# Kernel tuning notes

Measured on AMD Instinct MI355X. Metric: run time of the kernel, lower is better.

Reference implementation:

```python
import jax, jax.numpy as jnp
import numpy as np

D_MODEL = 1024
D_INNER = 2048      # expand * d_model
D_STATE = 64
HEADDIM = 128
NHEADS = 16         # d_inner // headdim
D_CONV = 4
CHUNK = 256
D_IN_PROJ = 2 * D_INNER + 2 * D_STATE + NHEADS   # 4240 (ngroups=1)
CONV_DIM = D_INNER + 2 * D_STATE                 # 2176
EPS = 1e-5


def setup_inputs() -> dict:
    key = jax.random.key(0)
    ks = jax.random.split(key, 8)
    B, L = 2, 4096
    u = jax.random.normal(ks[0], (B, L, D_MODEL), jnp.float32)
    in_proj_w = jax.random.normal(ks[1], (D_IN_PROJ, D_MODEL), jnp.float32) / np.sqrt(D_MODEL)
    conv_w = jax.random.uniform(ks[2], (CONV_DIM, D_CONV), jnp.float32, -0.5, 0.5)
    conv_b = jnp.zeros((CONV_DIM,), jnp.float32)
    # dt_bias init exactly as in the module: inv-softplus of dt ~ logU(1e-3, 1e-1)
    dt0 = jnp.exp(jax.random.uniform(ks[3], (NHEADS,), jnp.float32) * (np.log(0.1) - np.log(0.001)) + np.log(0.001))
    dt_bias = dt0 + jnp.log(-jnp.expm1(-dt0))
    A_log = jnp.log(jax.random.uniform(ks[4], (NHEADS,), jnp.float32, 1.0, 16.0))
    Dp = jnp.ones((NHEADS,), jnp.float32)
    norm_w = jnp.ones((D_INNER,), jnp.float32)
    out_proj_w = jax.random.normal(ks[5], (D_MODEL, D_INNER), jnp.float32) / np.sqrt(D_INNER)
    return dict(u=u, in_proj_w=in_proj_w, conv_w=conv_w, conv_b=conv_b, dt_bias=dt_bias,
                A_log=A_log, Dp=Dp, norm_w=norm_w, out_proj_w=out_proj_w)


def _ssd(x, dt, A, Bm, Cm, Dp):
    # Chunked selective state-space scan (mamba_chunk_scan_combined semantics).
    # x: [b,l,h,p], dt: [b,l,h] (already softplus'd), A: [h] (negative), Bm/Cm: [b,l,n]
    b, l, h, p = x.shape
    n = Bm.shape[-1]
    nc = l // CHUNK
    xc = x.reshape(b, nc, CHUNK, h, p)
    dtc = dt.reshape(b, nc, CHUNK, h)
    Bc = Bm.reshape(b, nc, CHUNK, n)
    Cc = Cm.reshape(b, nc, CHUNK, n)
    a = dtc * A                       # [b,c,q,h], a <= 0
    acum = jnp.cumsum(a, axis=2)      # within-chunk cumulative log-decay
    # ---- intra-chunk (causal, attention-like) ----
    scores = jnp.einsum('bcqn,bckn->bcqk', Cc, Bc)
    diff = acum[:, :, :, None, :] - acum[:, :, None, :, :]        # [b,c,q,k,h]
    mask = jnp.tril(jnp.ones((CHUNK, CHUNK), bool))[None, None, :, :, None]
    decay = jnp.exp(jnp.where(mask, diff, -jnp.inf))
    M = scores[..., None] * decay * dtc[:, :, None, :, :]         # [b,c,q,k,h]
    y_diag = jnp.einsum('bcqkh,bckhp->bcqhp', M, xc)
    # ---- per-chunk end states ----
    decay_states = jnp.exp(acum[:, :, -1:, :] - acum)             # [b,c,q,h]
    states = jnp.einsum('bcqh,bcqn,bcqhp->bchpn', dtc * decay_states, Bc, xc)
    # ---- inter-chunk recurrence (scan over nc chunks) ----
    chunk_decay = jnp.exp(acum[:, :, -1, :])                      # [b,c,h]
    def step(s, inp):
        st, cd = inp
        return cd[:, :, None, None] * s + st, s                   # emit state BEFORE this chunk
    init = jnp.zeros((b, h, p, n), x.dtype)
    _, prev = jax.lax.scan(step, init, (states.transpose(1, 0, 2, 3, 4), chunk_decay.transpose(1, 0, 2)))
    prev = prev.transpose(1, 0, 2, 3, 4)                          # [b,c,h,p,n]
    y_off = jnp.einsum('bcqn,bchpn,bcqh->bcqhp', Cc, prev, jnp.exp(acum))
    y = y_diag + y_off + xc * Dp[None, None, None, :, None]
    return y.reshape(b, l, h, p)


def _forward(u, in_proj_w, conv_w, conv_b, dt_bias, A_log, Dp, norm_w, out_proj_w):
    b, l, _ = u.shape
    zxbct = jnp.einsum('bld,ed->ble', u, in_proj_w)
    z = zxbct[..., :D_INNER]
    xBC = zxbct[..., D_INNER:D_INNER + CONV_DIM]
    dt = zxbct[..., D_INNER + CONV_DIM:]
    dt = jax.nn.softplus(dt + dt_bias)                            # [b,l,h]
    # causal depthwise conv1d (padding d_conv-1, truncated to seq_len) + SiLU
    xp = jnp.pad(xBC, ((0, 0), (D_CONV - 1, 0), (0, 0)))
    conv_out = conv_b
    for w in range(D_CONV):
        conv_out = conv_out + xp[:, w:w + l, :] * conv_w[:, w]
    xBC = jax.nn.silu(conv_out)
    x = xBC[..., :D_INNER]
    Bm = xBC[..., D_INNER:D_INNER + D_STATE]
    Cm = xBC[..., D_INNER + D_STATE:]
    A = -jnp.exp(A_log)
    y = _ssd(x.reshape(b, l, NHEADS, HEADDIM), dt, A, Bm, Cm, Dp)
    y = y.reshape(b, l, D_INNER)
    # RMSNormGated (norm_before_gate=False): gate first, then RMSNorm
    y = y * jax.nn.silu(z)
    y = y * jax.lax.rsqrt(jnp.mean(y * y, axis=-1, keepdims=True) + EPS) * norm_w
    return jnp.einsum('ble,de->bld', y, out_proj_w)


def reference(u, in_proj_w, conv_w, conv_b, dt_bias, A_log, Dp, norm_w, out_proj_w):
    return _forward(u, in_proj_w, conv_w, conv_b, dt_bias, A_log, Dp, norm_w, out_proj_w)
```

## Files before the change

kernel.cpp:

```cpp
#include <hip/hip_runtime.h>
#include <hip/hip_bf16.h>
#include <cstdint>
#include <cstddef>

#define D_MODEL   1024
#define D_INNER   2048
#define D_STATE   64
#define HEADDIM   128
#define NHEADS    16
#define D_CONV    4
#define CHUNK     256
#define D_IN_PROJ 4240
#define ZPAD      4352
#define CONV_DIM  2176
#define NB        2
#define LEN       4096
#define NC        16
#define MROWS     (NB*LEN)

typedef __hip_bfloat16 bf16;
typedef __bf16 bf16x8 __attribute__((ext_vector_type(8)));
typedef float  f32x4  __attribute__((ext_vector_type(4)));
typedef unsigned short us4 __attribute__((ext_vector_type(4)));

__device__ __forceinline__ float fsilu(float x){ return x / (1.f + __expf(-x)); }
__device__ __forceinline__ float toF(float x){ return x; }
__device__ __forceinline__ float toF(bf16 x){ return __bfloat162float(x); }

__device__ __forceinline__ unsigned short f2bs(float v){
  return __bfloat16_as_ushort(__float2bfloat16(v));
}
__device__ __forceinline__ void store4(bf16* p, f32x4 v){
  us4 o; o[0]=f2bs(v[0]); o[1]=f2bs(v[1]); o[2]=f2bs(v[2]); o[3]=f2bs(v[3]);
  *(us4*)p = o;
}
__device__ __forceinline__ void store4(float* p, f32x4 v){
  *(f32x4*)p = v;
}

__device__ __forceinline__ void gload_lds16(const void* g, void* l){
  __builtin_amdgcn_global_load_lds(
     (const __attribute__((address_space(1))) unsigned int*)(uintptr_t)g,
     (__attribute__((address_space(3))) unsigned int*)(uintptr_t)l, 16, 0, 0);
}

template<typename TC>
__global__ __launch_bounds__(512) void k_gemm_8w(
    const bf16* __restrict__ A, int lda,
    const bf16* __restrict__ B, int ldb,
    TC* __restrict__ C, int ldc, int K)
{
  __shared__ __align__(16) __bf16 As[2][128*64];
  __shared__ __align__(16) __bf16 Bs[2][128*64];
  const int tid  = threadIdx.x;
  const int w    = tid >> 6, l = tid & 63;
  const int quad = l >> 4, lq = l & 15;
  const int wm   = (w & 1)*64;
  const int wn   = (w >> 1)*32;
  const int m0 = blockIdx.x*128, n0 = blockIdx.y*128;

  const int sr = tid >> 3;
  const int sc = ((tid & 7) ^ (sr & 7)) * 8;
  const bf16* Ag = A + (size_t)(m0 + sr)*lda + sc;
  const bf16* Bg = B + (size_t)(n0 + sr)*ldb + sc;
  const int sdo = w*1024;

  auto stage = [&](int t, int buf){
    const int k0 = t*64;
    char* ab = (char*)&As[buf][0] + sdo;
    char* bb = (char*)&Bs[buf][0] + sdo;
    gload_lds16(Ag + k0,                  ab);
    gload_lds16(Ag + (size_t)64*lda + k0, ab + 8192);
    gload_lds16(Bg + k0,                  bb);
    gload_lds16(Bg + (size_t)64*ldb + k0, bb + 8192);
  };

  f32x4 acc[4][2] = {};

  stage(0, 0);
  const int NT = K >> 6;
  for (int t = 0; t < NT; ++t){
    const int cur = t & 1;
    if (t+1 < NT){
      stage(t+1, cur^1);
      asm volatile("s_waitcnt vmcnt(4)" ::: "memory");
    } else {
      asm volatile("s_waitcnt vmcnt(0)" ::: "memory");
    }
    asm volatile("s_barrier" ::: "memory");

    const char* Ab = (const char*)&As[cur][0];
    const char* Bb = (const char*)&Bs[cur][0];
    #pragma unroll
    for (int s=0;s<2;s++){
      const int slot = (((s*4 + quad) ^ (lq & 7)) << 4);
      bf16x8 af[4], bfr[2];
      #pragma unroll
      for (int tm=0;tm<4;tm++)
        af[tm]  = *(const bf16x8*)(Ab + (wm + tm*16 + lq)*128 + slot);
      #pragma unroll
      for (int tn=0;tn<2;tn++)
        bfr[tn] = *(const bf16x8*)(Bb + (wn + tn*16 + lq)*128 + slot);
      #pragma unroll
      for (int tm=0;tm<4;tm++)
        #pragma unroll
        for (int tn=0;tn<2;tn++)
          acc[tm][tn] = __builtin_amdgcn_mfma_f32_16x16x32_bf16(bfr[tn], af[tm], acc[tm][tn], 0,0,0);
    }
    asm volatile("s_barrier" ::: "memory");
  }

  #pragma unroll
  for (int tm = 0; tm < 4; tm++){
    int r = m0 + wm + tm*16 + lq;
    #pragma unroll
    for (int tn = 0; tn < 2; tn++){
      int cb = n0 + wn + tn*16 + quad*4;
      store4(&C[(size_t)r*ldc + cb], acc[tm][tn]);
    }
  }
}

template<typename TC>
__global__ __launch_bounds__(256) void k_gemm_db(
    const bf16* __restrict__ A, int lda,
    const bf16* __restrict__ B, int ldb,
    TC* __restrict__ C, int ldc, int K)
{
  __shared__ __align__(16) __bf16 As[2][128*64];
  __shared__ __align__(16) __bf16 Bs[2][128*64];
  const int tid  = threadIdx.x;
  const int w    = tid >> 6, l = tid & 63;
  const int quad = l >> 4, lq = l & 15;
  const int wm   = (w & 1)*64, wn = (w >> 1)*64;
  const int m0 = blockIdx.x*128, n0 = blockIdx.y*128;

  const int rs = w*8 + (l >> 3);
  const int cs = ((l & 7) ^ (l >> 3)) * 8;
  const bf16* Ag = A + (size_t)(m0 + rs)*lda + cs;
  const bf16* Bg = B + (size_t)(n0 + rs)*ldb + cs;

  auto stage = [&](int t, int buf){
    const int k0 = t*64;
    #pragma unroll
    for (int j=0;j<4;j++){
      gload_lds16(Ag + (size_t)j*32*lda + k0, (char*)&As[buf][0] + (j*32 + w*8)*128);
      gload_lds16(Bg + (size_t)j*32*ldb + k0, (char*)&Bs[buf][0] + (j*32 + w*8)*128);
    }
  };

  f32x4 acc[4][4] = {};

  stage(0, 0);
  const int NT = K >> 6;
  for (int t = 0; t < NT; ++t){
    const int cur = t & 1;
    if (t+1 < NT){
      stage(t+1, cur^1);
      asm volatile("s_waitcnt vmcnt(8)" ::: "memory");
    } else {
      asm volatile("s_waitcnt vmcnt(0)" ::: "memory");
    }
    asm volatile("s_barrier" ::: "memory");

    const char* Ab = (const char*)&As[cur][0];
    const char* Bb = (const char*)&Bs[cur][0];
    #pragma unroll
    for (int s=0;s<2;s++){
      const int slot = ((s*4 + quad) ^ (lq & 7)) << 4;
      bf16x8 af[4], bfr[4];
      #pragma unroll
      for (int tm=0;tm<4;tm++)
        af[tm]  = *(const bf16x8*)(Ab + (wm + lq + tm*16)*128 + slot);
      #pragma unroll
      for (int tn=0;tn<4;tn++)
        bfr[tn] = *(const bf16x8*)(Bb + (wn + lq + tn*16)*128 + slot);
      #pragma unroll
      for (int tm=0;tm<4;tm++)
        #pragma unroll
        for (int tn=0;tn<4;tn++)
          acc[tm][tn] = __builtin_amdgcn_mfma_f32_16x16x32_bf16(bfr[tn], af[tm], acc[tm][tn], 0,0,0);
    }
    asm volatile("s_barrier" ::: "memory");
  }

  #pragma unroll
  for (int tm = 0; tm < 4; tm++){
    int r = m0 + wm + tm*16 + lq;
    #pragma unroll
    for (int tn = 0; tn < 4; tn++){
      int cb = n0 + wn + tn*16 + quad*4;
      store4(&C[(size_t)r*ldc + cb], acc[tm][tn]);
    }
  }
}

#define NU4  (MROWS*D_MODEL/4)
#define NW14 (ZPAD*D_MODEL/4)
#define NW24 (D_MODEL*D_INNER/4)
__global__ __launch_bounds__(256) void k_convert(
    const float* __restrict__ u, const float* __restrict__ Win,
    const float* __restrict__ Wout, const float* __restrict__ norm_w,
    bf16* __restrict__ ub, bf16* __restrict__ Wb_in, bf16* __restrict__ Wb_out){
  int i4 = blockIdx.x*256 + threadIdx.x;
  if (i4 < NU4){
    float4 v = ((const float4*)u)[i4];
    us4 o = {f2bs(v.x), f2bs(v.y), f2bs(v.z), f2bs(v.w)};
    ((us4*)ub)[i4] = o;
  } else if (i4 < NU4 + NW14){
    int j = i4 - NU4;
    int r = j >> 8;
    float4 v = make_float4(0.f,0.f,0.f,0.f);
    if (r < D_IN_PROJ) v = ((const float4*)Win)[j];
    us4 o = {f2bs(v.x), f2bs(v.y), f2bs(v.z), f2bs(v.w)};
    ((us4*)Wb_in)[j] = o;
  } else {
    int j = i4 - NU4 - NW14;
    float4 v = ((const float4*)Wout)[j];
    float4 nw = ((const float4*)norm_w)[j & 511];
    us4 o = {f2bs(v.x*nw.x), f2bs(v.y*nw.y), f2bs(v.z*nw.z), f2bs(v.w*nw.w)};
    ((us4*)Wb_out)[j] = o;
  }
}

__global__ __launch_bounds__(256) void k_dt(
    const bf16* __restrict__ zxbct, const float* __restrict__ dt_bias,
    const float* __restrict__ A_log, float* __restrict__ dt_t,
    float* __restrict__ acum_t, float* __restrict__ cd_t){
  int bid = blockIdx.x;
  int h = bid & 15, c = (bid>>4)&15, b = bid>>8;
  int q = threadIdx.x;
  size_t m = (size_t)(b*NC + c)*CHUNK + q;
  float x = toF(zxbct[m*ZPAD + (D_INNER + CONV_DIM) + h]) + dt_bias[h];
  float dtv = (x > 20.f) ? x : log1pf(__expf(x));
  float Ah = -__expf(A_log[h]);
  float a = dtv * Ah;
  __shared__ float sb[CHUNK];
  sb[q] = a;
  __syncthreads();
  #pragma unroll
  for (int off=1; off<CHUNK; off<<=1){
    float t = (q >= off) ? sb[q-off] : 0.f;
    __syncthreads();
    sb[q] += t;
    __syncthreads();
  }
  float ac = sb[q];
  size_t o = ((size_t)(b*NHEADS+h))*LEN + c*CHUNK + q;
  dt_t[o]   = dtv;
  acum_t[o] = ac;
  if (q == CHUNK-1) cd_t[(b*NHEADS+h)*NC + c] = __expf(ac);
}

__global__ __launch_bounds__(256) void k_conv(
    const bf16* __restrict__ zxbct, const float* __restrict__ conv_w,
    const float* __restrict__ conv_b, bf16* __restrict__ xbc){
  __shared__ __align__(16) __bf16 xs[67*64];
  __shared__ __align__(16) float  ws[64*4];
  __shared__ float bs[64];
  const int tid = threadIdx.x;
  const int cq = tid & 7;
  const int tm = tid >> 3;
  const int c0 = blockIdx.x*64;
  const int m0 = blockIdx.y*64;
  {
    int g = m0 - 3 + tm; if (g < 0) g = 0;
    *(bf16x8*)&xs[tm*64 + cq*8] =
        *(const bf16x8*)(zxbct + (size_t)g*ZPAD + D_INNER + c0 + cq*8);
    int g2 = m0 - 3 + tm + 32;
    *(bf16x8*)&xs[(tm+32)*64 + cq*8] =
        *(const bf16x8*)(zxbct + (size_t)g2*ZPAD + D_INNER + c0 + cq*8);
    if (tid < 24){
      int r3 = 64 + (tid >> 3);
      int g3 = m0 - 3 + r3;
      *(bf16x8*)&xs[r3*64 + cq*8] =
          *(const bf16x8*)(zxbct + (size_t)g3*ZPAD + D_INNER + c0 + cq*8);
    }
  }
  if (tid < 64)      *(float4*)&ws[tid*4] = *(const float4*)(conv_w + (size_t)(c0+tid)*4);
  else if (tid < 128) bs[tid-64] = conv_b[c0 + tid - 64];
  __syncthreads();

  #pragma unroll
  for (int rr=0; rr<2; rr++){
    const int r = tm + rr*32;
    const int m = m0 + r;
    const int l = m & (LEN-1);
    float acc[8];
    #pragma unroll
    for (int j=0;j<8;j++) acc[j] = bs[cq*8+j];
    #pragma unroll
    for (int w=0; w<D_CONV; w++){
      if (l - (D_CONV-1) + w >= 0){
        bf16x8 v = *(const bf16x8*)&xs[(r+w)*64 + cq*8];
        #pragma unroll
        for (int j=0;j<8;j++) acc[j] += (float)v[j] * ws[(cq*8+j)*4 + w];
      }
    }
    bf16x8 o;
    #pragma unroll
    for (int j=0;j<8;j++) o[j] = (__bf16)fsilu(acc[j]);
    *(bf16x8*)(xbc + (size_t)m*CONV_DIM + c0 + cq*8) = o;
  }
}

__global__ __launch_bounds__(256,2) void k_states(
    const bf16* __restrict__ xbc, const float* __restrict__ acum_t,
    const float* __restrict__ dt_t, float* __restrict__ states)
{
  const int bid = blockIdx.x;
  const int h = bid & 15, c = (bid>>4)&15, b = bid>>8;
  const int z = b*NC + c;
  const int tid = threadIdx.x;
  const int w = tid >> 6, l = tid & 63;
  const int quad = l >> 4, lq = l & 15;

  __shared__ __align__(16) __bf16 xsT[2][128*72];
  __shared__ __align__(16) __bf16 bts[2][64*72];

  const float* acum = acum_t + ((size_t)(b*NHEADS+h))*LEN + c*CHUNK;
  const float* dtc  = dt_t   + ((size_t)(b*NHEADS+h))*LEN + c*CHUNK;
  const float alast = acum[CHUNK-1];
  const bf16* xrow = xbc + (size_t)z*CHUNK*CONV_DIM + h*HEADDIM;
  const bf16* Brow = xbc + (size_t)z*CHUNK*CONV_DIM + D_INNER;

  f32x4 Sst[2][4] = {};

  auto stage = [&](int t, int buf){
    const int k0 = t*64;
    const bf16* xr = xrow + (size_t)(k0+l)*CONV_DIM;
    #pragma unroll
    for (int pass=0; pass<4; pass++){
      int pb = w*8 + pass*32;
      bf16x8 v = *(const bf16x8*)(xr + pb);
      #pragma unroll
      for (int j=0;j<8;j++) xsT[buf][(pb+j)*72 + l] = v[j];
    }
    float wl = dtc[k0+l] * __expf(alast - acum[k0+l]);
    const bf16* br = Brow + (size_t)(k0+l)*CONV_DIM;
    #pragma unroll
    for (int pass=0; pass<2; pass++){
      int nb = w*8 + pass*32;
      bf16x8 v = *(const bf16x8*)(br + nb);
      #pragma unroll
      for (int j=0;j<8;j++) bts[buf][(nb+j)*72 + l] = (__bf16)((float)v[j] * wl);
    }
  };

  stage(0, 0);
  for (int t = 0; t < 4; t++){
    const int buf = t & 1;
    __syncthreads();
    if (t < 3) stage(t+1, buf^1);
    #pragma unroll
    for (int s=0;s<2;s++){
      bf16x8 a2[2];
      #pragma unroll
      for (int mi=0;mi<2;mi++)
        a2[mi] = *(const bf16x8*)&xsT[buf][(w*32 + mi*16 + lq)*72 + s*32 + quad*8];
      #pragma unroll
      for (int ni=0;ni<4;ni++){
        bf16x8 bb = *(const bf16x8*)&bts[buf][(ni*16+lq)*72 + s*32 + quad*8];
        #pragma unroll
        for (int mi=0;mi<2;mi++)
          Sst[mi][ni] = __builtin_amdgcn_mfma_f32_16x16x32_bf16(bb, a2[mi], Sst[mi][ni], 0,0,0);
      }
    }
  }

  float* so = states + (size_t)bid*HEADDIM*D_STATE;
  #pragma unroll
  for (int mi=0;mi<2;mi++){
    int pp = w*32 + mi*16 + lq;
    #pragma unroll
    for (int ni=0;ni<4;ni++)
      store4(&so[pp*D_STATE + ni*16 + quad*4], Sst[mi][ni]);
  }
}

__global__ __launch_bounds__(256) void k_scan(
    const float* __restrict__ states, const float* __restrict__ cd_t,
    bf16* __restrict__ prevb){
  int b = blockIdx.x >> 4, h = blockIdx.x & 15;
  int pt = blockIdx.y;
  int tid = threadIdx.x;
  float carry[4] = {0.f,0.f,0.f,0.f};
  for (int c=0;c<NC;c++){
    size_t base = ((size_t)(b*256 + c*16 + h))*HEADDIM*D_STATE + (size_t)pt*1024;
    float cd = cd_t[(b*NHEADS+h)*NC + c];
    #pragma unroll
    for (int i=0;i<4;i++){
      size_t idx = base + (size_t)i*256 + tid;
      prevb[idx] = __float2bfloat16(carry[i]);
      carry[i] = carry[i]*cd + states[idx];
    }
  }
}

__global__ __launch_bounds__(256,2) void k_fused(
    const bf16* __restrict__ xbc, const float* __restrict__ acum_t,
    const float* __restrict__ dt_t, const float* __restrict__ Dp,
    const bf16* __restrict__ prevb, bf16* __restrict__ y)
{
  const int bid = blockIdx.x;
  const int h = bid & 15, c = (bid>>4)&15, b = bid>>8;
  const int z = b*NC + c;
  const int tid = threadIdx.x;
  const int w = tid >> 6, l = tid & 63;
  const int quad = l >> 4, lq = l & 15;

  __shared__ __align__(16) __bf16 xsT[2][128*72];
  __shared__ __align__(16) __bf16 Ms[4][32*40];
  __shared__ float acs[CHUNK], dts[CHUNK];

  const float* acum = acum_t + ((size_t)(b*NHEADS+h))*LEN + c*CHUNK;
  const float* dtc  = dt_t   + ((size_t)(b*NHEADS+h))*LEN + c*CHUNK;
  acs[tid] = acum[tid];
  dts[tid] = dtc[tid];

  const bf16* xrow = xbc + (size_t)z*CHUNK*CONV_DIM + h*HEADDIM;
  const bf16* Brow = xbc + (size_t)z*CHUNK*CONV_DIM + D_INNER;
  const bf16* Crow = xbc + (size_t)z*CHUNK*CONV_DIM + D_INNER + D_STATE;
  const bf16* pv   = prevb + (size_t)bid*HEADDIM*D_STATE;
  const float Dph = Dp[h];
  const int j0 = w, j1 = 7 - w;

  f32x4 Yacc[2][2][8] = {};

  auto stage = [&](int t, int buf){
    const bf16* xr = xrow + (size_t)(t*64+l)*CONV_DIM;
    #pragma unroll
    for (int pass=0; pass<4; pass++){
      int pb = w*8 + pass*32;
      bf16x8 v = *(const bf16x8*)(xr + pb);
      #pragma unroll
      for (int j=0;j<8;j++) xsT[buf][(pb+j)*72 + l] = v[j];
    }
  };

  stage(0, 0);
  __syncthreads();

  #pragma unroll
  for (int s=0;s<2;s++){
    bf16x8 bp[8];
    #pragma unroll
    for (int pn=0;pn<8;pn++)
      bp[pn] = *(const bf16x8*)(pv + (pn*16+lq)*D_STATE + s*32 + quad*8);
    #pragma unroll
    for (int half=0; half<2; half++){
      const int j = half ? j1 : j0;
      #pragma unroll
      for (int qm=0;qm<2;qm++){
        int row = j*32 + qm*16 + lq;
        float e = __expf(acs[row]);
        bf16x8 a = *(const bf16x8*)(Crow + (size_t)row*CONV_DIM + s*32 + quad*8);
        bf16x8 ae;
        #pragma unroll
        for (int jj=0;jj<8;jj++) ae[jj] = (__bf16)((float)a[jj] * e);
        #pragma unroll
        for (int pn=0;pn<8;pn++)
          Yacc[half][qm][pn] = __builtin_amdgcn_mfma_f32_16x16x32_bf16(bp[pn], ae, Yacc[half][qm][pn], 0,0,0);
      }
    }
  }

  for (int t = 0; t < 4; t++){
    const int buf = t & 1;
    if (t > 0) __syncthreads();
    if (t < 3) stage(t+1, buf^1);

    #pragma unroll
    for (int half=0; half<2; half++){
      const int j = half ? j1 : j0;
      if (2*t > j) continue;
      const int qbase = j*32;
      bf16x8 cf[2][2];
      #pragma unroll
      for (int s=0;s<2;s++)
        #pragma unroll
        for (int qm=0;qm<2;qm++)
          cf[s][qm] = *(const bf16x8*)(Crow + (size_t)(qbase+qm*16+lq)*CONV_DIM + s*32 + quad*8);
      #pragma unroll
      for (int kk=0; kk<2; kk++){
        const int kh = 2*t + kk;
        if (kh > j) continue;
        const int kb32  = kk*32;
        const int kbase = kh*32;
        f32x4 Sacc[2][2] = {};
        #pragma unroll
        for (int s=0;s<2;s++){
          bf16x8 bfk[2];
          #pragma unroll
          for (int kn=0;kn<2;kn++)
            bfk[kn] = *(const bf16x8*)(Brow + (size_t)(kbase+kn*16+lq)*CONV_DIM + s*32 + quad*8);
          #pragma unroll
          for (int kn=0;kn<2;kn++)
            #pragma unroll
            for (int qm=0;qm<2;qm++)
              Sacc[kn][qm] = __builtin_amdgcn_mfma_f32_16x16x32_bf16(bfk[kn], cf[s][qm], Sacc[kn][qm], 0,0,0);
        }
        #pragma unroll
        for (int qm=0;qm<2;qm++){
          int ql = qbase + qm*16 + lq;
          float aq = acs[ql];
          #pragma unroll
          for (int kn=0;kn<2;kn++){
            us4 o;
            #pragma unroll
            for (int i=0;i<4;i++){
              int kl = kbase + kn*16 + quad*4 + i;
              float v = Sacc[kn][qm][i] * __expf(aq - acs[kl]) * dts[kl];
              v = (kl < ql) ? v : ((kl == ql) ? v + Dph : 0.f);
              o[i] = f2bs(v);
            }
            *(us4*)&Ms[w][(qm*16+lq)*40 + kn*16 + quad*4] = o;
          }
        }
        asm volatile("s_waitcnt lgkmcnt(0)" ::: "memory");
        #pragma unroll
        for (int qm=0;qm<2;qm++){
          bf16x8 am = *(const bf16x8*)&Ms[w][(qm*16+lq)*40 + quad*8];
          #pragma unroll
          for (int pn=0;pn<8;pn++){
            bf16x8 bp = *(const bf16x8*)&xsT[buf][(pn*16+lq)*72 + kb32 + quad*8];
            Yacc[half][qm][pn] = __builtin_amdgcn_mfma_f32_16x16x32_bf16(bp, am, Yacc[half][qm][pn], 0,0,0);
          }
        }
      }
    }
  }

  bf16* yrow = y + (size_t)z*CHUNK*D_INNER + h*HEADDIM;
  #pragma unroll
  for (int half=0; half<2; half++){
    const int j = half ? j1 : j0;
    #pragma unroll
    for (int qm=0;qm<2;qm++){
      int q = j*32 + qm*16 + lq;
      #pragma unroll
      for (int pn=0;pn<8;pn++)
        store4(&yrow[(size_t)q*D_INNER + pn*16 + quad*4], Yacc[half][qm][pn]);
    }
  }
}

__global__ __launch_bounds__(256) void k_gatenorm(
    const bf16* __restrict__ zxbct, bf16* __restrict__ y){
  int m = blockIdx.x;
  int e0 = threadIdx.x*8;
  bf16x8 zv = *(const bf16x8*)(zxbct + (size_t)m*ZPAD + e0);
  bf16x8 yv = *(const bf16x8*)(y + (size_t)m*D_INNER + e0);
  float v[8]; float ss = 0.f;
  #pragma unroll
  for (int j=0;j<8;j++){
    float val = (float)yv[j] * fsilu((float)zv[j]);
    v[j] = val; ss += val*val;
  }
  #pragma unroll
  for (int off=32; off>0; off>>=1) ss += __shfl_down(ss, off, 64);
  __shared__ float red[4];
  if ((threadIdx.x & 63) == 0) red[threadIdx.x >> 6] = ss;
  __syncthreads();
  float tot = red[0]+red[1]+red[2]+red[3];
  float r = rsqrtf(tot * (1.f/D_INNER) + 1e-5f);
  bf16x8 o;
  #pragma unroll
  for (int j=0;j<8;j++) o[j] = (__bf16)(v[j] * r);
  *(bf16x8*)(y + (size_t)m*D_INNER + e0) = o;
}

extern "C" void kernel_launch(void* const* d_in, const int* in_sizes, int n_in,
                              void* d_out, int out_size, void* d_ws, size_t ws_size,
                              hipStream_t stream) {
  const float* u         = (const float*)d_in[0];
  const float* in_proj_w = (const float*)d_in[1];
  const float* conv_w    = (const float*)d_in[2];
  const float* conv_b    = (const float*)d_in[3];
  const float* dt_bias   = (const float*)d_in[4];
  const float* A_log     = (const float*)d_in[5];
  const float* Dp        = (const float*)d_in[6];
  const float* norm_w    = (const float*)d_in[7];
  const float* out_proj_w= (const float*)d_in[8];
  float* out = (float*)d_out;

  char* p = (char*)d_ws;
  auto alloc = [&](size_t bytes){ char* r = p; p += (bytes + 255) & ~size_t(255); return r; };
  bf16*  zxbct = (bf16*) alloc((size_t)MROWS*ZPAD*2);
  bf16*  xbc   = (bf16*) alloc((size_t)MROWS*CONV_DIM*2);
  bf16*  y     = (bf16*) alloc((size_t)MROWS*D_INNER*2);
  bf16*  ub    = (bf16*) alloc((size_t)MROWS*D_MODEL*2);
  bf16*  Wb_in = (bf16*) alloc((size_t)ZPAD*D_MODEL*2);
  bf16*  Wb_out= (bf16*) alloc((size_t)D_MODEL*D_INNER*2);
  float* dt_t  = (float*)alloc((size_t)NB*NHEADS*LEN*4);
  float* acum_t= (float*)alloc((size_t)NB*NHEADS*LEN*4);
  float* cd_t  = (float*)alloc((size_t)NB*NHEADS*NC*4);
  float* states= (float*)ub;
  bf16*  prevb = (bf16*)Wb_in;

  dim3 blk(256);
  k_convert<<<dim3((NU4+NW14+NW24)/256), blk, 0, stream>>>(
      u, in_proj_w, out_proj_w, norm_w, ub, Wb_in, Wb_out);

  k_gemm_8w<bf16><<<dim3(64, 34), dim3(512), 0, stream>>>(
      ub, D_MODEL, Wb_in, D_MODEL, zxbct, ZPAD, D_MODEL);

  k_dt    <<<dim3(NB*NC*NHEADS), blk, 0, stream>>>(zxbct, dt_bias, A_log, dt_t, acum_t, cd_t);
  k_conv  <<<dim3(CONV_DIM/64, MROWS/64), blk, 0, stream>>>(zxbct, conv_w, conv_b, xbc);
  k_states<<<dim3(NB*NC*NHEADS), blk, 0, stream>>>(xbc, acum_t, dt_t, states);
  k_scan  <<<dim3(NB*NHEADS, 8), blk, 0, stream>>>(states, cd_t, prevb);
  k_fused <<<dim3(NB*NC*NHEADS), blk, 0, stream>>>(xbc, acum_t, dt_t, Dp, prevb, y);
  k_gatenorm<<<dim3(MROWS), blk, 0, stream>>>(zxbct, y);

  k_gemm_db<float><<<dim3(64, 8), blk, 0, stream>>>(
      y, D_INNER, Wb_out, D_INNER, out, D_MODEL, D_INNER);
}
```

Before: 339.6 us.

## Enlarge in_proj GEMM tile to 256x128 with 16 waves and K-step 32

Replaces the 8-wave 128x128 in_proj GEMM with a 16-wave 1024-thread kernel computing 256x128 tiles. The K step shrinks from 64 to 32, and the LDS layout and swizzle are reworked so two rows share a 128-byte line. Only the first 512 threads load B. The goal is more reuse of each B tile and fewer blocks, at the cost of twice as many barrier iterations, less latency hiding per stage, and lower occupancy per block.

```diff
diff --git a/kernel.cpp b/kernel.cpp
--- a/kernel.cpp
+++ b/kernel.cpp
@@ -45,68 +45,65 @@
 }
 
 template<typename TC>
-__global__ __launch_bounds__(512) void k_gemm_8w(
+__global__ __launch_bounds__(1024) void k_gemm_16w(
     const bf16* __restrict__ A, int lda,
     const bf16* __restrict__ B, int ldb,
     TC* __restrict__ C, int ldc, int K)
 {
-  __shared__ __align__(16) __bf16 As[2][128*64];
-  __shared__ __align__(16) __bf16 Bs[2][128*64];
+  __shared__ __align__(16) __bf16 As[2][256*32];
+  __shared__ __align__(16) __bf16 Bs[2][128*32];
   const int tid  = threadIdx.x;
   const int w    = tid >> 6, l = tid & 63;
   const int quad = l >> 4, lq = l & 15;
-  const int wm   = (w & 1)*64;
-  const int wn   = (w >> 1)*32;
-  const int m0 = blockIdx.x*128, n0 = blockIdx.y*128;
-
-  const int sr = tid >> 3;
-  const int sc = ((tid & 7) ^ (sr & 7)) * 8;
+  const int wm   = (w & 3)*64;
+  const int wn   = (w >> 2)*32;
+  const int m0 = blockIdx.x*256, n0 = blockIdx.y*128;
+
+  const int sr = ((tid >> 3) << 1) | ((tid >> 2) & 1);
+  const int sc = ((tid & 3) ^ ((tid >> 3) & 3)) * 8;
   const bf16* Ag = A + (size_t)(m0 + sr)*lda + sc;
   const bf16* Bg = B + (size_t)(n0 + sr)*ldb + sc;
   const int sdo = w*1024;
 
   auto stage = [&](int t, int buf){
-    const int k0 = t*64;
-    char* ab = (char*)&As[buf][0] + sdo;
-    char* bb = (char*)&Bs[buf][0] + sdo;
-    gload_lds16(Ag + k0,                  ab);
-    gload_lds16(Ag + (size_t)64*lda + k0, ab + 8192);
-    gload_lds16(Bg + k0,                  bb);
-    gload_lds16(Bg + (size_t)64*ldb + k0, bb + 8192);
+    const int k0 = t*32;
+    gload_lds16(Ag + k0, (char*)&As[buf][0] + sdo);
+    if (tid < 512)
+      gload_lds16(Bg + k0, (char*)&Bs[buf][0] + sdo);
   };
 
+  auto lread = [&](const __bf16* base, int row)->bf16x8 {
+    const int p = row >> 1;
+    const int byte = p*128 + (row & 1)*64 + ((quad ^ (p & 3)) << 4);
+    return *(const bf16x8*)((const char*)base + byte);
+  };
+
   f32x4 acc[4][2] = {};
 
   stage(0, 0);
-  const int NT = K >> 6;
+  const int NT = K >> 5;
   for (int t = 0; t < NT; ++t){
     const int cur = t & 1;
     if (t+1 < NT){
       stage(t+1, cur^1);
-      asm volatile("s_waitcnt vmcnt(4)" ::: "memory");
+      if (w < 8) { asm volatile("s_waitcnt vmcnt(2)" ::: "memory"); }
+      else       { asm volatile("s_waitcnt vmcnt(1)" ::: "memory"); }
     } else {
       asm volatile("s_waitcnt vmcnt(0)" ::: "memory");
     }
     asm volatile("s_barrier" ::: "memory");
 
-    const char* Ab = (const char*)&As[cur][0];
-    const char* Bb = (const char*)&Bs[cur][0];
-    #pragma unroll
-    for (int s=0;s<2;s++){
-      const int slot = (((s*4 + quad) ^ (lq & 7)) << 4);
-      bf16x8 af[4], bfr[2];
-      #pragma unroll
-      for (int tm=0;tm<4;tm++)
-        af[tm]  = *(const bf16x8*)(Ab + (wm + tm*16 + lq)*128 + slot);
+    bf16x8 af[4], bfr[2];
+    #pragma unroll
+    for (int tm=0;tm<4;tm++) af[tm]  = lread(&As[cur][0], wm + tm*16 + lq);
+    #pragma unroll
+    for (int tn=0;tn<2;tn++) bfr[tn] = lread(&Bs[cur][0], wn + tn*16 + lq);
+    #pragma unroll
+    for (int tm=0;tm<4;tm++)
       #pragma unroll
       for (int tn=0;tn<2;tn++)
-        bfr[tn] = *(const bf16x8*)(Bb + (wn + tn*16 + lq)*128 + slot);
-      #pragma unroll
-      for (int tm=0;tm<4;tm++)
-        #pragma unroll
-        for (int tn=0;tn<2;tn++)
-          acc[tm][tn] = __builtin_amdgcn_mfma_f32_16x16x32_bf16(bfr[tn], af[tm], acc[tm][tn], 0,0,0);
-    }
+        acc[tm][tn] = __builtin_amdgcn_mfma_f32_16x16x32_bf16(bfr[tn], af[tm], acc[tm][tn], 0,0,0);
+
     asm volatile("s_barrier" ::: "memory");
   }
 
@@ -602,7 +599,7 @@
   k_convert<<<dim3((NU4+NW14+NW24)/256), blk, 0, stream>>>(
       u, in_proj_w, out_proj_w, norm_w, ub, Wb_in, Wb_out);
 
-  k_gemm_8w<bf16><<<dim3(64, 34), dim3(512), 0, stream>>>(
+  k_gemm_16w<bf16><<<dim3(32, 34), dim3(1024), 0, stream>>>(
       ub, D_MODEL, Wb_in, D_MODEL, zxbct, ZPAD, D_MODEL);
 
   k_dt    <<<dim3(NB*NC*NHEADS), blk, 0, stream>>>(zxbct, dt_bias, A_log, dt_t, acum_t, cd_t);
```

Result: slower. 359.1 us (+5.7%).
